# Performance work log

Hardware: AMD Instinct MI355X
Metric: run time of the kernel (lower is better)

Reference implementation:

```python
import jax, jax.numpy as jnp
import numpy as np
import math

HIDDEN = 1024
HEADS = 16
HEAD_DIM = HIDDEN // HEADS


def setup_inputs() -> dict:
    key = jax.random.key(0)
    ks = jax.random.split(key, 9)
    s = 1.0 / math.sqrt(HIDDEN)
    x = jax.random.normal(ks[0], (4, 2048, HIDDEN), dtype=jnp.float32)
    Wq = jax.random.uniform(ks[1], (HIDDEN, HIDDEN), jnp.float32, -s, s)
    bq = jax.random.uniform(ks[2], (HIDDEN,), jnp.float32, -s, s)
    Wk = jax.random.uniform(ks[3], (HIDDEN, HIDDEN), jnp.float32, -s, s)
    bk = jax.random.uniform(ks[4], (HIDDEN,), jnp.float32, -s, s)
    Wv = jax.random.uniform(ks[5], (HIDDEN, HIDDEN), jnp.float32, -s, s)
    bv = jax.random.uniform(ks[6], (HIDDEN,), jnp.float32, -s, s)
    Wo = jax.random.uniform(ks[7], (HIDDEN, HIDDEN), jnp.float32, -s, s)
    bo = jax.random.uniform(ks[8], (HIDDEN,), jnp.float32, -s, s)
    return {"x": x, "Wq": Wq, "bq": bq, "Wk": Wk, "bk": bk,
            "Wv": Wv, "bv": bv, "Wo": Wo, "bo": bo}


def reference(x, Wq, bq, Wk, bk, Wv, bv, Wo, bo):
    B, T, D = x.shape
    H, Hd = HEADS, HEAD_DIM
    scale = 1.0 / math.sqrt(Hd)
    # projections (torch Linear: y = x @ W.T + b)
    q = (x @ Wq.T + bq).reshape(B, T, H, Hd).transpose(0, 2, 1, 3)  # [B,H,T,Hd]
    k = (x @ Wk.T + bk).reshape(B, T, H, Hd).transpose(0, 2, 1, 3)
    v = (x @ Wv.T + bv).reshape(B, T, H, Hd).transpose(0, 2, 1, 3)
    scores = jnp.einsum("bhqd,bhkd->bhqk", q, k) * scale  # [B,H,T,T]
    attn = jax.nn.softmax(scores, axis=-1)
    out = jnp.einsum("bhqk,bhkd->bhqd", attn, v)  # [B,H,T,Hd]
    out = out.transpose(0, 2, 1, 3).reshape(B, T, D)
    out = out @ Wo.T + bo
    return out.mean(axis=1)  # [B, D]
```

## Files before the change

kernel.cpp:

```cpp
#include <hip/hip_runtime.h>
#include <stdint.h>

#define HIDDEN 1024
#define HEADS 16
#define HEAD_DIM 64
#define BATCH 4
#define SEQ 2048
#define NTOK (BATCH * SEQ)

typedef __attribute__((ext_vector_type(8))) short bf16x8;
typedef __attribute__((ext_vector_type(4))) float floatx4;
typedef __attribute__((ext_vector_type(16))) float floatx16;

#define SCALE_Q 0.18033688011112042f

__device__ __forceinline__ unsigned short f2bf(float f) {
    union { float f; unsigned u; } x; x.f = f;
    unsigned r = x.u + 0x7fffu + ((x.u >> 16) & 1u);
    return (unsigned short)(r >> 16);
}

__device__ __forceinline__ float fast_exp2(float x) {
#if __has_builtin(__builtin_amdgcn_exp2f)
    return __builtin_amdgcn_exp2f(x);
#else
    return exp2f(x);
#endif
}

typedef __attribute__((address_space(3))) unsigned int lds_u32;
typedef const __attribute__((address_space(1))) unsigned int gl_u32;

__device__ __forceinline__ void async_cp16(const void* g, void* l) {
#if __has_builtin(__builtin_amdgcn_global_load_lds)
    __builtin_amdgcn_global_load_lds((gl_u32*)g, (lds_u32*)l, 16, 0, 0);
#else
    *(uint4*)((char*)l + (threadIdx.x & 63) * 16) = *(const uint4*)g;
#endif
}

__global__ __launch_bounds__(256) void conv_all(
    const float* __restrict__ x, const float* __restrict__ Wq,
    const float* __restrict__ Wk, const float* __restrict__ Wv,
    unsigned short* __restrict__ x_bf, unsigned short* __restrict__ wq_bf,
    unsigned short* __restrict__ wk_bf, unsigned short* __restrict__ wv_bf,
    float* __restrict__ accp) {
    const int blk = blockIdx.x, tid = threadIdx.x;
    const float* src;
    unsigned short* dst;
    size_t i;
    if (blk < 8192) {
        src = x; dst = x_bf; i = (size_t)blk * 256 + tid;
        if (blk < 16) accp[blk * 256 + tid] = 0.0f;
    } else {
        int r = blk - 8192;
        int s = r >> 10;
        src = (s == 0) ? Wq : (s == 1) ? Wk : Wv;
        dst = (s == 0) ? wq_bf : (s == 1) ? wk_bf : wv_bf;
        i = (size_t)(r & 1023) * 256 + tid;
    }
    float4 v = *(const float4*)(src + 4 * i);
    unsigned short o[4];
    o[0] = f2bf(v.x); o[1] = f2bf(v.y); o[2] = f2bf(v.z); o[3] = f2bf(v.w);
    *(ushort4*)(dst + 4 * i) = *(ushort4*)o;
}

__global__ __launch_bounds__(256, 3) void qkv_gemm(
    const unsigned short* __restrict__ X,
    const unsigned short* __restrict__ W0, const unsigned short* __restrict__ W1,
    const unsigned short* __restrict__ W2,
    const float* __restrict__ b0, const float* __restrict__ b1,
    const float* __restrict__ b2,
    unsigned short* __restrict__ O0, unsigned short* __restrict__ O1,
    unsigned short* __restrict__ O2) {
    __shared__ __align__(16) char smem[34816];
    unsigned short* tbuf = (unsigned short*)smem;

    const int id = blockIdx.x;
    const int mb = id & 63, nzb = id >> 6;
    const int z = nzb >> 3, nz = nzb & 7;
    const int m0 = mb * 128;
    const unsigned short* W = (z == 0) ? W0 : (z == 1) ? W1 : W2;
    const float* bias       = (z == 0) ? b0 : (z == 1) ? b1 : b2;

    const int tid = threadIdx.x, lane = tid & 63, wave = tid >> 6;
    const int wm = (wave & 1) * 64, wn = (wave >> 1) * 64;

    const int srow = lane >> 2;
    const int sxc = ((lane & 3) ^ (srow & 3)) * 8;
    const unsigned short* ga[2];
    const unsigned short* gb[2];
#pragma unroll
    for (int j = 0; j < 2; ++j) {
        ga[j] = X + (size_t)(m0 + wave * 32 + j * 16 + srow) * HIDDEN + sxc;
        gb[j] = W + (size_t)(nz * 128 + wave * 32 + j * 16 + srow) * HIDDEN + sxc;
    }

    floatx4 acc[4][4];
#pragma unroll
    for (int tm = 0; tm < 4; ++tm)
#pragma unroll
        for (int tn = 0; tn < 4; ++tn)
#pragma unroll
            for (int r = 0; r < 4; ++r) acc[tm][tn][r] = 0.f;

#pragma unroll
    for (int j = 0; j < 2; ++j) {
        async_cp16(ga[j], smem + wave * 2048 + j * 1024);
        async_cp16(gb[j], smem + 16384 + wave * 2048 + j * 1024);
        ga[j] += 32; gb[j] += 32;
    }
    __syncthreads();

    const int fr = (lane & 15) * 64 + (((lane >> 4) ^ (lane & 3)) * 16);
    for (int kt = 0; kt < 32; ++kt) {
        const int cur = kt & 1;
        if (kt < 31) {
#pragma unroll
            for (int j = 0; j < 2; ++j) {
                async_cp16(ga[j], smem + (cur ^ 1) * 8192 + wave * 2048 + j * 1024);
                async_cp16(gb[j], smem + 16384 + (cur ^ 1) * 8192 + wave * 2048 + j * 1024);
                ga[j] += 32; gb[j] += 32;
            }
        }
        const char* Ab = smem + cur * 8192;
        const char* Bb = smem + 16384 + cur * 8192;
        bf16x8 af[4], bfr[4];
#pragma unroll
        for (int t = 0; t < 4; ++t) {
            af[t]  = *(bf16x8*)(Ab + (wm + t * 16) * 64 + fr);
            bfr[t] = *(bf16x8*)(Bb + (wn + t * 16) * 64 + fr);
        }
#pragma unroll
        for (int tm = 0; tm < 4; ++tm)
#pragma unroll
            for (int tn = 0; tn < 4; ++tn)
                acc[tm][tn] = __builtin_amdgcn_mfma_f32_16x16x32_bf16(af[tm], bfr[tn], acc[tm][tn], 0, 0, 0);
        if (kt < 31) __syncthreads();
    }

    const int col = lane & 15, rbase = (lane >> 4) * 4;
    __syncthreads();
    if (z == 2) {
#pragma unroll
        for (int tm = 0; tm < 4; ++tm)
#pragma unroll
            for (int tn = 0; tn < 4; ++tn) {
                const int dr = wn + tn * 16 + col;
                const float bs = bias[nz * 128 + dr];
                const int mi0 = wm + tm * 16 + rbase;
                const int mip = (mi0 & ~12) | ((mi0 & 4) << 1) | ((mi0 & 8) >> 1);
                unsigned short vals[4];
#pragma unroll
                for (int r = 0; r < 4; ++r) vals[r] = f2bf(acc[tm][tn][r] + bs);
                *(ushort4*)&tbuf[dr * 136 + mip] = *(ushort4*)vals;
            }
        __syncthreads();
        const int dr = tid >> 1, seg = tid & 1;
        const int hh = nz * 2 + (dr >> 6), dd = dr & 63;
        const int bb = m0 >> 11, tb = (m0 & (SEQ - 1)) >> 7;
        unsigned short* dst = O2 + (((size_t)bb * HEADS + hh) * HEAD_DIM + dd) * SEQ
                                 + tb * 128 + seg * 64;
        const unsigned short* srcl = &tbuf[dr * 136 + seg * 64];
#pragma unroll
        for (int i = 0; i < 8; ++i)
            *(uint4*)(dst + i * 8) = *(const uint4*)(srcl + i * 8);
    } else {
        unsigned short* O = (z == 0) ? O0 : O1;
        const float sc = (z == 0) ? SCALE_Q : 1.0f;
#pragma unroll
        for (int tm = 0; tm < 4; ++tm)
#pragma unroll
            for (int tn = 0; tn < 4; ++tn) {
                const int nn = wn + tn * 16 + col;
                const float bs = bias[nz * 128 + nn];
                const int mi0 = wm + tm * 16 + rbase;
#pragma unroll
                for (int r = 0; r < 4; ++r)
                    tbuf[(mi0 + r) * 136 + nn] = f2bf((acc[tm][tn][r] + bs) * sc);
            }
        __syncthreads();
        const int r = tid >> 1, seg = tid & 1;
        unsigned short* dst = O + (size_t)(m0 + r) * HIDDEN + nz * 128 + seg * 64;
        const unsigned short* srcl = &tbuf[r * 136 + seg * 64];
#pragma unroll
        for (int i = 0; i < 8; ++i)
            *(uint4*)(dst + i * 8) = *(const uint4*)(srcl + i * 8);
    }
}

__global__ __launch_bounds__(256, 4) void attn_mfma(
    const unsigned short* __restrict__ Q, const unsigned short* __restrict__ K,
    const unsigned short* __restrict__ Vt, float* __restrict__ accp) {
    __shared__ unsigned short Klds[2][4096];
    __shared__ unsigned short Vlds[2][4096];

    const int tid = threadIdx.x, lane = tid & 63, wave = tid >> 6;
    const int lq = lane & 31, g2 = lane >> 5;

    const int f = blockIdx.x;
    const int bh = (f & 7) * 8 + ((f >> 3) & 7);
    const int qc = f >> 6;
    const int b = bh >> 4, h = bh & 15;

    bf16x8 qfrag[4];
    {
        const size_t qb = ((size_t)(b * SEQ + qc * 128 + wave * 32 + lq)) * HIDDEN
                          + h * HEAD_DIM + g2 * 8;
#pragma unroll
        for (int ds = 0; ds < 4; ++ds) qfrag[ds] = *(const bf16x8*)&Q[qb + ds * 16];
    }

    const unsigned short* kg[2];
    const unsigned short* vg[2];
    {
        const int kr = lane >> 3;
        const int kc = ((lane & 7) ^ kr) * 8;
#pragma unroll
        for (int j = 0; j < 2; ++j)
            kg[j] = K + ((size_t)(b * SEQ + wave * 16 + j * 8 + kr)) * HIDDEN + h * HEAD_DIM + kc;
#pragma unroll
        for (int j = 0; j < 2; ++j) {
            const int dl = wave * 16 + j * 8 + (lane >> 3);
            const int cc = ((lane & 7) ^ (dl & 7)) * 8;
            vg[j] = Vt + ((size_t)bh * HEAD_DIM + dl) * SEQ + cc;
        }
    }

    floatx16 oacc[2];
#pragma unroll
    for (int r = 0; r < 16; ++r) { oacc[0][r] = 0.f; oacc[1][r] = 0.f; }
    float lsum0 = 0.f, lsum1 = 0.f;

#pragma unroll
    for (int j = 0; j < 2; ++j) {
        async_cp16(kg[j], (char*)Klds[0] + (wave * 16 + j * 8) * 128);
        async_cp16(vg[j], (char*)Vlds[0] + (wave * 16 + j * 8) * 128);
        kg[j] += 64 * HIDDEN; vg[j] += 64;
    }
    __syncthreads();

    for (int it = 0; it < 32; ++it) {
        const int cur = it & 1;
        if (it < 31) {
#pragma unroll
            for (int j = 0; j < 2; ++j) {
                async_cp16(kg[j], (char*)Klds[cur ^ 1] + (wave * 16 + j * 8) * 128);
                async_cp16(vg[j], (char*)Vlds[cur ^ 1] + (wave * 16 + j * 8) * 128);
                kg[j] += 64 * HIDDEN; vg[j] += 64;
            }
        }
#pragma unroll
        for (int s32 = 0; s32 < 2; ++s32) {
            const int rr = s32 * 32 + lq;
            bf16x8 kf[4];
#pragma unroll
            for (int ds = 0; ds < 4; ++ds)
                kf[ds] = *(bf16x8*)((char*)Klds[cur] + rr * 128 + (((g2 + 2 * ds) ^ (lq & 7)) * 16));

            floatx16 sacc;
#pragma unroll
            for (int r = 0; r < 16; ++r) sacc[r] = 0.f;
            __builtin_amdgcn_s_setprio(1);
#pragma unroll
            for (int ds = 0; ds < 4; ++ds)
                sacc = __builtin_amdgcn_mfma_f32_32x32x16_bf16(kf[ds], qfrag[ds], sacc, 0, 0, 0);
            __builtin_amdgcn_s_setprio(0);

            unsigned pk[8];
#pragma unroll
            for (int j = 0; j < 8; ++j) {
                union { float f; unsigned u; } plo, phi;
                plo.f = fast_exp2(sacc[2 * j]);
                phi.f = fast_exp2(sacc[2 * j + 1]);
                lsum0 += plo.f;
                lsum1 += phi.f;
                pk[j] = __builtin_amdgcn_perm(phi.u, plo.u, 0x07060302u);
            }
#pragma unroll
            for (int ks2 = 0; ks2 < 2; ++ks2) {
                const int s = s32 * 2 + ks2;
                bf16x8 vf[2];
#pragma unroll
                for (int nf = 0; nf < 2; ++nf) {
                    const int d = nf * 32 + lq;
                    const int c = (2 * s + g2) ^ (d & 7);
                    vf[nf] = *(bf16x8*)((char*)Vlds[cur] + d * 128 + c * 16);
                }
                union { uint4 u; bf16x8 v; } af;
                af.u.x = pk[4 * ks2];
                af.u.y = pk[4 * ks2 + 1];
                af.u.z = pk[4 * ks2 + 2];
                af.u.w = pk[4 * ks2 + 3];
                __builtin_amdgcn_s_setprio(1);
#pragma unroll
                for (int nf = 0; nf < 2; ++nf)
                    oacc[nf] = __builtin_amdgcn_mfma_f32_32x32x16_bf16(af.v, vf[nf], oacc[nf], 0, 0, 0);
                __builtin_amdgcn_s_setprio(0);
            }
        }
        if (it < 31) __syncthreads();
    }

    float lfull = lsum0 + lsum1;
    lfull += __shfl_xor(lfull, 32, 64);
    float linv[16];
#pragma unroll
    for (int r = 0; r < 16; ++r) {
        const int qr = (r & 3) + 8 * (r >> 2) + 4 * g2;
        linv[r] = 1.0f / __shfl(lfull, qr, 64);
    }
#pragma unroll
    for (int nf = 0; nf < 2; ++nf) {
        float v = 0.f;
#pragma unroll
        for (int r = 0; r < 16; ++r) v += oacc[nf][r] * linv[r];
        v += __shfl_xor(v, 32, 64);
        if (lane < 32)
            atomicAdd(&accp[b * HIDDEN + h * HEAD_DIM + nf * 32 + lq], v);
    }
}

__global__ __launch_bounds__(256) void out_proj(const float* __restrict__ acc,
                                                const float* __restrict__ Wo,
                                                const float* __restrict__ bo,
                                                float* __restrict__ out) {
    __shared__ float red[256];
    const int n = blockIdx.x * 64 + (threadIdx.x & 63);
    const int ks = threadIdx.x >> 6;
    const int b = blockIdx.y;
    const float* wr = Wo + (size_t)n * HIDDEN + ks * 256;
    const float* ar = acc + b * HIDDEN + ks * 256;
    float s = 0.f;
#pragma unroll 8
    for (int k = 0; k < 256; k += 4) {
        float4 w = *(const float4*)(wr + k);
        float4 a = *(const float4*)(ar + k);
        s += w.x * a.x + w.y * a.y + w.z * a.z + w.w * a.w;
    }
    red[threadIdx.x] = s;
    __syncthreads();
    if (threadIdx.x < 64) {
        float t = red[threadIdx.x] + red[threadIdx.x + 64]
                + red[threadIdx.x + 128] + red[threadIdx.x + 192];
        out[b * HIDDEN + n] = t * (1.0f / (float)SEQ) + bo[n];
    }
}

extern "C" void kernel_launch(void* const* d_in, const int* in_sizes, int n_in,
                              void* d_out, int out_size, void* d_ws, size_t ws_size,
                              hipStream_t stream) {
    const float* x  = (const float*)d_in[0];
    const float* Wq = (const float*)d_in[1];
    const float* bq = (const float*)d_in[2];
    const float* Wk = (const float*)d_in[3];
    const float* bk = (const float*)d_in[4];
    const float* Wv = (const float*)d_in[5];
    const float* bv = (const float*)d_in[6];
    const float* Wo = (const float*)d_in[7];
    const float* bo = (const float*)d_in[8];
    float* out = (float*)d_out;

    char* ws = (char*)d_ws;
    unsigned short* x_bf  = (unsigned short*)(ws);
    unsigned short* wq_bf = (unsigned short*)(ws + 16777216);
    unsigned short* wk_bf = (unsigned short*)(ws + 18874368);
    unsigned short* wv_bf = (unsigned short*)(ws + 20971520);
    unsigned short* q_bf  = (unsigned short*)(ws + 23068672);
    unsigned short* k_bf  = (unsigned short*)(ws + 39845888);
    unsigned short* vt_bf = (unsigned short*)(ws + 56623104);
    float*          accp  = (float*)(ws + 73400320);

    conv_all<<<dim3(8192 + 3072), dim3(256), 0, stream>>>(
        x, Wq, Wk, Wv, x_bf, wq_bf, wk_bf, wv_bf, accp);

    qkv_gemm<<<dim3(1536), dim3(256), 0, stream>>>(
        x_bf, wq_bf, wk_bf, wv_bf, bq, bk, bv, q_bf, k_bf, vt_bf);

    attn_mfma<<<dim3(1024), dim3(256), 0, stream>>>(q_bf, k_bf, vt_bf, accp);

    out_proj<<<dim3(16, BATCH), dim3(256), 0, stream>>>(accp, Wo, bo, out);
}
```

Measured before the change: 252.7 us.

## Process two 32-row query groups per wave in attention to reuse K/V tiles

Each wave in the attention kernel now handles 64 query rows as two 32-row groups. Each K/V tile loaded into LDS is reused for twice as many queries, and the grid is halved to 512 blocks. This cuts global and LDS traffic for K and V per query. In exchange it doubles the accumulator and query-fragment registers, which is why launch bounds drop from 4 to 2 blocks per CU, and fewer blocks may leave parts of the 256 CUs underused.

```diff
diff --git a/kernel.cpp b/kernel.cpp
--- a/kernel.cpp
+++ b/kernel.cpp
@@ -189,7 +189,7 @@
     }
 }
 
-__global__ __launch_bounds__(256, 4) void attn_mfma(
+__global__ __launch_bounds__(256, 2) void attn_mfma(
     const unsigned short* __restrict__ Q, const unsigned short* __restrict__ K,
     const unsigned short* __restrict__ Vt, float* __restrict__ accp) {
     __shared__ unsigned short Klds[2][4096];
@@ -203,12 +203,13 @@
     const int qc = f >> 6;
     const int b = bh >> 4, h = bh & 15;
 
-    bf16x8 qfrag[4];
-    {
-        const size_t qb = ((size_t)(b * SEQ + qc * 128 + wave * 32 + lq)) * HIDDEN
+    bf16x8 qfrag[2][4];
+#pragma unroll
+    for (int grp = 0; grp < 2; ++grp) {
+        const size_t qb = ((size_t)(b * SEQ + qc * 256 + wave * 64 + grp * 32 + lq)) * HIDDEN
                           + h * HEAD_DIM + g2 * 8;
 #pragma unroll
-        for (int ds = 0; ds < 4; ++ds) qfrag[ds] = *(const bf16x8*)&Q[qb + ds * 16];
+        for (int ds = 0; ds < 4; ++ds) qfrag[grp][ds] = *(const bf16x8*)&Q[qb + ds * 16];
     }
 
     const unsigned short* kg[2];
@@ -227,10 +228,13 @@
         }
     }
 
-    floatx16 oacc[2];
-#pragma unroll
-    for (int r = 0; r < 16; ++r) { oacc[0][r] = 0.f; oacc[1][r] = 0.f; }
-    float lsum0 = 0.f, lsum1 = 0.f;
+    floatx16 oacc[2][2];
+#pragma unroll
+    for (int r = 0; r < 16; ++r) {
+        oacc[0][0][r] = 0.f; oacc[0][1][r] = 0.f;
+        oacc[1][0][r] = 0.f; oacc[1][1][r] = 0.f;
+    }
+    float lsum00 = 0.f, lsum01 = 0.f, lsum10 = 0.f, lsum11 = 0.f;
 
 #pragma unroll
     for (int j = 0; j < 2; ++j) {
@@ -258,24 +262,27 @@
             for (int ds = 0; ds < 4; ++ds)
                 kf[ds] = *(bf16x8*)((char*)Klds[cur] + rr * 128 + (((g2 + 2 * ds) ^ (lq & 7)) * 16));
 
-            floatx16 sacc;
-#pragma unroll
-            for (int r = 0; r < 16; ++r) sacc[r] = 0.f;
-            __builtin_amdgcn_s_setprio(1);
-#pragma unroll
-            for (int ds = 0; ds < 4; ++ds)
-                sacc = __builtin_amdgcn_mfma_f32_32x32x16_bf16(kf[ds], qfrag[ds], sacc, 0, 0, 0);
-            __builtin_amdgcn_s_setprio(0);
-
-            unsigned pk[8];
-#pragma unroll
-            for (int j = 0; j < 8; ++j) {
-                union { float f; unsigned u; } plo, phi;
-                plo.f = fast_exp2(sacc[2 * j]);
-                phi.f = fast_exp2(sacc[2 * j + 1]);
-                lsum0 += plo.f;
-                lsum1 += phi.f;
-                pk[j] = __builtin_amdgcn_perm(phi.u, plo.u, 0x07060302u);
+            unsigned pk[2][8];
+#pragma unroll
+            for (int grp = 0; grp < 2; ++grp) {
+                floatx16 sacc;
+#pragma unroll
+                for (int r = 0; r < 16; ++r) sacc[r] = 0.f;
+                __builtin_amdgcn_s_setprio(1);
+#pragma unroll
+                for (int ds = 0; ds < 4; ++ds)
+                    sacc = __builtin_amdgcn_mfma_f32_32x32x16_bf16(kf[ds], qfrag[grp][ds], sacc, 0, 0, 0);
+                __builtin_amdgcn_s_setprio(0);
+
+#pragma unroll
+                for (int j = 0; j < 8; ++j) {
+                    union { float f; unsigned u; } plo, phi;
+                    plo.f = fast_exp2(sacc[2 * j]);
+                    phi.f = fast_exp2(sacc[2 * j + 1]);
+                    if (grp == 0) { lsum00 += plo.f; lsum01 += phi.f; }
+                    else          { lsum10 += plo.f; lsum11 += phi.f; }
+                    pk[grp][j] = __builtin_amdgcn_perm(phi.u, plo.u, 0x07060302u);
+                }
             }
 #pragma unroll
             for (int ks2 = 0; ks2 < 2; ++ks2) {
@@ -287,34 +294,41 @@
                     const int c = (2 * s + g2) ^ (d & 7);
                     vf[nf] = *(bf16x8*)((char*)Vlds[cur] + d * 128 + c * 16);
                 }
-                union { uint4 u; bf16x8 v; } af;
-                af.u.x = pk[4 * ks2];
-                af.u.y = pk[4 * ks2 + 1];
-                af.u.z = pk[4 * ks2 + 2];
-                af.u.w = pk[4 * ks2 + 3];
-                __builtin_amdgcn_s_setprio(1);
-#pragma unroll
-                for (int nf = 0; nf < 2; ++nf)
-                    oacc[nf] = __builtin_amdgcn_mfma_f32_32x32x16_bf16(af.v, vf[nf], oacc[nf], 0, 0, 0);
-                __builtin_amdgcn_s_setprio(0);
+#pragma unroll
+                for (int grp = 0; grp < 2; ++grp) {
+                    union { uint4 u; bf16x8 v; } af;
+                    af.u.x = pk[grp][4 * ks2];
+                    af.u.y = pk[grp][4 * ks2 + 1];
+                    af.u.z = pk[grp][4 * ks2 + 2];
+                    af.u.w = pk[grp][4 * ks2 + 3];
+                    __builtin_amdgcn_s_setprio(1);
+#pragma unroll
+                    for (int nf = 0; nf < 2; ++nf)
+                        oacc[grp][nf] = __builtin_amdgcn_mfma_f32_32x32x16_bf16(af.v, vf[nf], oacc[grp][nf], 0, 0, 0);
+                    __builtin_amdgcn_s_setprio(0);
+                }
             }
         }
         if (it < 31) __syncthreads();
     }
 
-    float lfull = lsum0 + lsum1;
-    lfull += __shfl_xor(lfull, 32, 64);
-    float linv[16];
-#pragma unroll
-    for (int r = 0; r < 16; ++r) {
-        const int qr = (r & 3) + 8 * (r >> 2) + 4 * g2;
-        linv[r] = 1.0f / __shfl(lfull, qr, 64);
+    float linv[2][16];
+#pragma unroll
+    for (int grp = 0; grp < 2; ++grp) {
+        float lf = (grp == 0) ? (lsum00 + lsum01) : (lsum10 + lsum11);
+        lf += __shfl_xor(lf, 32, 64);
+#pragma unroll
+        for (int r = 0; r < 16; ++r) {
+            const int qr = (r & 3) + 8 * (r >> 2) + 4 * g2;
+            linv[grp][r] = 1.0f / __shfl(lf, qr, 64);
+        }
     }
 #pragma unroll
     for (int nf = 0; nf < 2; ++nf) {
         float v = 0.f;
 #pragma unroll
-        for (int r = 0; r < 16; ++r) v += oacc[nf][r] * linv[r];
+        for (int r = 0; r < 16; ++r)
+            v += oacc[0][nf][r] * linv[0][r] + oacc[1][nf][r] * linv[1][r];
         v += __shfl_xor(v, 32, 64);
         if (lane < 32)
             atomicAdd(&accp[b * HIDDEN + h * HEAD_DIM + nf * 32 + lq], v);
@@ -377,7 +391,7 @@
     qkv_gemm<<<dim3(1536), dim3(256), 0, stream>>>(
         x_bf, wq_bf, wk_bf, wv_bf, bq, bk, bv, q_bf, k_bf, vt_bf);
 
-    attn_mfma<<<dim3(1024), dim3(256), 0, stream>>>(q_bf, k_bf, vt_bf, accp);
+    attn_mfma<<<dim3(512), dim3(256), 0, stream>>>(q_bf, k_bf, vt_bf, accp);
 
     out_proj<<<dim3(16, BATCH), dim3(256), 0, stream>>>(accp, Wo, bo, out);
 }
```

New measurement: 250.1 us. Within noise of the previous version (-1.0%).
